# Kernel optimization log

Hardware: AMD Instinct MI355X
Metric: run time of the kernel (lower is better)

Reference implementation:

```python
import jax, jax.numpy as jnp
import numpy as np

B, N, D, H, E = 128, 256, 256, 8, 524288
RATIO = 0.5
HD = D // H
K_SEL = int(N * RATIO)  # nodes kept per graph


def setup_inputs() -> dict:
    key = jax.random.key(0)
    ks = jax.random.split(key, 12)
    embeddings = jax.random.normal(ks[0], (B, N, D), dtype=jnp.float32)
    mask = jnp.ones((B, N), dtype=bool)
    dist = jax.random.uniform(ks[1], (B, N, N), dtype=jnp.float32)
    # within-graph random edges, offset per graph
    epg = E // B
    src = jax.random.randint(ks[2], (B, epg), 0, N)
    dst = jax.random.randint(ks[3], (B, epg), 0, N)
    off = (jnp.arange(B) * N)[:, None]
    edge_index = jnp.stack([(src + off).reshape(-1), (dst + off).reshape(-1)]).astype(jnp.int64)
    batch = jnp.repeat(jnp.arange(B, dtype=jnp.int64), N)
    s = 1.0 / np.sqrt(D)
    Wq = jax.random.normal(ks[4], (D, D), jnp.float32) * s
    Wk = jax.random.normal(ks[5], (D, D), jnp.float32) * s
    Wv = jax.random.normal(ks[6], (D, D), jnp.float32) * s
    Wo = jax.random.normal(ks[7], (D, D), jnp.float32) * s
    bq = jnp.zeros((D,), jnp.float32)
    bk = jnp.zeros((D,), jnp.float32)
    bv = jnp.zeros((D,), jnp.float32)
    bo = jnp.zeros((D,), jnp.float32)
    pool_w = jax.random.normal(ks[8], (D,), jnp.float32) * s
    return dict(embeddings=embeddings, mask=mask, dist=dist, edge_index=edge_index,
                batch=batch, Wq=Wq, bq=bq, Wk=Wk, bk=bk, Wv=Wv, bv=bv, Wo=Wo, bo=bo,
                pool_w=pool_w)


def _mha(x, mask, dist, Wq, bq, Wk, bk, Wv, bv, Wo, bo):
    # x: [B,N,D]; dist used as additive attention bias; mask: [B,N] key mask
    q = (x @ Wq + bq).reshape(B, N, H, HD).transpose(0, 2, 1, 3)  # bhnd
    k = (x @ Wk + bk).reshape(B, N, H, HD).transpose(0, 2, 1, 3)
    v = (x @ Wv + bv).reshape(B, N, H, HD).transpose(0, 2, 1, 3)
    scores = jnp.einsum('bhnd,bhmd->bhnm', q, k) / jnp.sqrt(jnp.float32(HD))
    scores = scores + dist[:, None]  # broadcast bias over heads
    scores = jnp.where(mask[:, None, None, :], scores, jnp.float32(-1e9))
    attn = jax.nn.softmax(scores, axis=-1)
    out = jnp.einsum('bhnm,bhmd->bhnd', attn, v)
    out = out.transpose(0, 2, 1, 3).reshape(B, N, D)
    return out @ Wo + bo


def reference(embeddings, mask, dist, edge_index, batch, Wq, bq, Wk, bk, Wv, bv, Wo, bo, pool_w):
    encoder_result = _mha(embeddings, mask, dist, Wq, bq, Wk, bk, Wv, bv, Wo, bo)
    # encoder_result[mask] -> sparse node features; mask is all-true so shape is [B*N, D]
    x = encoder_result.reshape(B * N, D)

    # ---- TopKPooling (PyG semantics): score = x.w/||w||, keep top ceil(ratio*N)/graph ----
    score = (x @ pool_w) / jnp.linalg.norm(pool_w)          # [B*N]
    vals, idx = jax.lax.top_k(score.reshape(B, N), K_SEL)    # per-graph top-k
    perm = (idx + (jnp.arange(B) * N)[:, None]).reshape(-1)  # [B*K] global node ids
    sub_x = x[perm] * jnp.tanh(vals).reshape(-1, 1)
    sub_batch = batch[perm]

    # relabel nodes: new id = position in perm (PyG ordering); dropped -> sentinel
    n_keep = B * K_SEL
    sentinel = n_keep
    new_id = jnp.full((B * N,), sentinel, dtype=edge_index.dtype).at[perm].set(
        jnp.arange(n_keep, dtype=edge_index.dtype))
    row = new_id[edge_index[0]]
    col = new_id[edge_index[1]]
    valid = (row < sentinel) & (col < sentinel)
    row = jnp.where(valid, row, sentinel)
    col = jnp.where(valid, col, sentinel)
    # sort_edge_index: row-major sort; invalid (sentinel) edges pushed to the end
    order = jnp.argsort(row * (sentinel + 1) + col)
    sub_edge_index = jnp.stack([row, col])[:, order]
    return encoder_result, sub_x, sub_edge_index, sub_batch
```

## Files before the change

kernel.cpp:

```cpp
#include <hip/hip_runtime.h>
#include <math.h>

#define Bg   128
#define Ng   256
#define Dg   256
#define Hg   8
#define HDg  32
#define Eg   524288
#define Kg   128
#define BNg  32768
#define SENT 16384

using bf16x8 = __attribute__((ext_vector_type(8))) short;
using f32x4  = __attribute__((ext_vector_type(4))) float;

__device__ inline void split2(float x, short &h, short &l) {
    unsigned u = __float_as_uint(x);
    h = (short)(u >> 16);
    float hf = __uint_as_float(u & 0xffff0000u);
    float r = x - hf;
    l = (short)(__float_as_uint(r) >> 16);
}
__device__ inline unsigned pack2(short a, short b) {
    return (unsigned)(unsigned short)a | ((unsigned)(unsigned short)b << 16);
}

__global__ __launch_bounds__(256) void split_x(
    const float* __restrict__ x, short* __restrict__ xh, short* __restrict__ xl)
{
    size_t i = ((size_t)blockIdx.x * 256 + threadIdx.x) * 8;
    float4 a = *(const float4*)(x + i);
    float4 b = *(const float4*)(x + i + 4);
    float v[8] = {a.x,a.y,a.z,a.w,b.x,b.y,b.z,b.w};
    short h[8], l[8];
    #pragma unroll
    for (int j = 0; j < 8; ++j) split2(v[j], h[j], l[j]);
    uint4 uh, ul;
    uh.x = pack2(h[0],h[1]); uh.y = pack2(h[2],h[3]);
    uh.z = pack2(h[4],h[5]); uh.w = pack2(h[6],h[7]);
    ul.x = pack2(l[0],l[1]); ul.y = pack2(l[2],l[3]);
    ul.z = pack2(l[4],l[5]); ul.w = pack2(l[6],l[7]);
    *(uint4*)(xh + i) = uh;
    *(uint4*)(xl + i) = ul;
}

__global__ __launch_bounds__(256) void wprep(
    const float* __restrict__ Wq, const float* __restrict__ Wk,
    const float* __restrict__ Wv, const float* __restrict__ Wo,
    short* __restrict__ WTh, short* __restrict__ WTl)
{
    __shared__ float t[64][65];
    const int bid = blockIdx.x;
    const int mat = bid >> 4;
    const int kt = (bid >> 2) & 3, nt = bid & 3;
    const float* W = (mat==0) ? Wq : (mat==1) ? Wk : (mat==2) ? Wv : Wo;
    const int tid = threadIdx.x;
    const int r = tid >> 2, c4 = tid & 3;
    #pragma unroll
    for (int i = 0; i < 4; ++i) {
        float4 v = *(const float4*)(W + (size_t)(kt*64 + r)*256 + nt*64 + c4*16 + i*4);
        t[r][c4*16 + i*4 + 0] = v.x; t[r][c4*16 + i*4 + 1] = v.y;
        t[r][c4*16 + i*4 + 2] = v.z; t[r][c4*16 + i*4 + 3] = v.w;
    }
    __syncthreads();
    const int n = r, k0 = c4 * 16;
    short hb[16], lb[16];
    #pragma unroll
    for (int i = 0; i < 16; ++i) split2(t[k0 + i][n], hb[i], lb[i]);
    size_t base = (size_t)mat*65536 + (size_t)(nt*64 + n)*256 + kt*64 + k0;
    uint4 uh0, uh1, ul0, ul1;
    uh0.x=pack2(hb[0],hb[1]);  uh0.y=pack2(hb[2],hb[3]);  uh0.z=pack2(hb[4],hb[5]);  uh0.w=pack2(hb[6],hb[7]);
    uh1.x=pack2(hb[8],hb[9]);  uh1.y=pack2(hb[10],hb[11]);uh1.z=pack2(hb[12],hb[13]);uh1.w=pack2(hb[14],hb[15]);
    ul0.x=pack2(lb[0],lb[1]);  ul0.y=pack2(lb[2],lb[3]);  ul0.z=pack2(lb[4],lb[5]);  ul0.w=pack2(lb[6],lb[7]);
    ul1.x=pack2(lb[8],lb[9]);  ul1.y=pack2(lb[10],lb[11]);ul1.z=pack2(lb[12],lb[13]);ul1.w=pack2(lb[14],lb[15]);
    *(uint4*)&WTh[base]     = uh0; *(uint4*)&WTh[base + 8] = uh1;
    *(uint4*)&WTl[base]     = ul0; *(uint4*)&WTl[base + 8] = ul1;
}

__global__ __launch_bounds__(256) void qkv_mm(
    const short* __restrict__ xh, const short* __restrict__ xl,
    const short* __restrict__ WTh, const short* __restrict__ WTl,
    const float* __restrict__ bq, const float* __restrict__ bk, const float* __restrict__ bv,
    short* __restrict__ Qh, short* __restrict__ Ql,
    short* __restrict__ Kh, short* __restrict__ Kl,
    short* __restrict__ Vh, short* __restrict__ Vl)
{
    const int z = blockIdx.z;
    const float* bias = (z==0) ? bq : (z==1) ? bk : bv;
    short* outH       = (z==0) ? Qh : (z==1) ? Kh : Vh;
    short* outL       = (z==0) ? Ql : (z==1) ? Kl : Vl;
    const float scale = (z==0) ? 0.17677669529663687f : 1.0f;
    const short* bth = WTh + (size_t)z * 65536;
    const short* btl = WTl + (size_t)z * 65536;
    __shared__ __align__(16) short lds[16384];
    const int tid = threadIdx.x;
    const int lane = tid & 63, w = tid >> 6;
    const int g = lane >> 4, li = lane & 15;
    const int wr = w >> 1, wc = w & 1;
    const int m0 = blockIdx.x * 128, n0 = blockIdx.y * 128;
    f32x4 acc[4][4];
    #pragma unroll
    for (int i = 0; i < 4; ++i)
        #pragma unroll
        for (int j = 0; j < 4; ++j) acc[i][j] = (f32x4){0.f,0.f,0.f,0.f};

    for (int k0 = 0; k0 < 256; k0 += 32) {
        #pragma unroll
        for (int it = 0; it < 2; ++it) {
            int chunk = it*256 + tid;
            int r = chunk >> 2, c = chunk & 3;
            size_t ga = (size_t)(m0 + r)*256 + k0 + c*8;
            size_t gb = (size_t)(n0 + r)*256 + k0 + c*8;
            uint4 vh = *(const uint4*)(xh + ga);
            uint4 vl = *(const uint4*)(xl + ga);
            uint4 wh = *(const uint4*)(bth + gb);
            uint4 wl = *(const uint4*)(btl + gb);
            *(uint4*)&lds[        chunk*8] = vh;
            *(uint4*)&lds[ 4096 + chunk*8] = vl;
            *(uint4*)&lds[ 8192 + chunk*8] = wh;
            *(uint4*)&lds[12288 + chunk*8] = wl;
        }
        __syncthreads();
        bf16x8 ah[4], al[4], bh[4], bl[4];
        #pragma unroll
        for (int i = 0; i < 4; ++i) {
            int row = wr*64 + i*16 + li;
            ah[i] = *(const bf16x8*)&lds[       row*32 + g*8];
            al[i] = *(const bf16x8*)&lds[4096 + row*32 + g*8];
        }
        #pragma unroll
        for (int j = 0; j < 4; ++j) {
            int row = wc*64 + j*16 + li;
            bh[j] = *(const bf16x8*)&lds[ 8192 + row*32 + g*8];
            bl[j] = *(const bf16x8*)&lds[12288 + row*32 + g*8];
        }
        #pragma unroll
        for (int i = 0; i < 4; ++i)
            #pragma unroll
            for (int j = 0; j < 4; ++j) {
                acc[i][j] = __builtin_amdgcn_mfma_f32_16x16x32_bf16(ah[i], bh[j], acc[i][j], 0,0,0);
                acc[i][j] = __builtin_amdgcn_mfma_f32_16x16x32_bf16(ah[i], bl[j], acc[i][j], 0,0,0);
                acc[i][j] = __builtin_amdgcn_mfma_f32_16x16x32_bf16(al[i], bh[j], acc[i][j], 0,0,0);
            }
        __syncthreads();
    }
    #pragma unroll
    for (int i = 0; i < 4; ++i)
        #pragma unroll
        for (int j = 0; j < 4; ++j)
            #pragma unroll
            for (int r = 0; r < 4; ++r) {
                int m = m0 + wr*64 + i*16 + g*4 + r;
                int c = n0 + wc*64 + j*16 + li;
                int b = m >> 8, nn = m & 255;
                int h = c >> 5, hd = c & 31;
                float val = (acc[i][j][r] + bias[c]) * scale;
                short hh, ll; split2(val, hh, ll);
                size_t idx = ((size_t)(b*Hg + h)*Ng + nn)*HDg + hd;
                outH[idx] = hh; outL[idx] = ll;
            }
}

__global__ __launch_bounds__(512, 4) void attn_mfma(
    const short* __restrict__ Qh, const short* __restrict__ Ql,
    const short* __restrict__ Kh, const short* __restrict__ Kl,
    const short* __restrict__ Vh, const short* __restrict__ Vl,
    const float* __restrict__ dist,
    short* __restrict__ AOh, short* __restrict__ AOl)
{
    __shared__ __align__(16) short Khi [2][32][40];
    __shared__ __align__(16) short Klo [2][32][40];
    __shared__ __align__(16) short Vthi[2][32][40];
    __shared__ __align__(16) short Vtlo[2][32][40];
    __shared__ __align__(16) short Phi [8][32][40];
    __shared__ __align__(16) short Plo [8][32][40];

    const int i0 = blockIdx.x;
    const int xcd = i0 & 7;
    const int m_  = i0 >> 3;
    const int h   = m_ & 7;
    const int b   = (m_ >> 3) * 8 + xcd;
    const int bh  = b * 8 + h;

    const int tid = threadIdx.x;
    const int w = tid >> 6;
    const int lane = tid & 63;
    const int g = lane >> 4;
    const int li = lane & 15;
    const int q0 = w * 32;
    const int skey = tid >> 4;
    const int se0  = (tid & 15) * 2;
    const float* dall = dist + (size_t)b*Ng*Ng;

    bf16x8 qh[2], ql[2];
    #pragma unroll
    for (int tq = 0; tq < 2; ++tq) {
        size_t qoff = ((size_t)bh * Ng + q0 + tq*16 + li) * HDg + g*8;
        qh[tq] = *(const bf16x8*)(Qh + qoff);
        ql[tq] = *(const bf16x8*)(Ql + qoff);
    }

    {
        size_t koff = ((size_t)bh*Ng + skey) * HDg + se0;
        unsigned kh1 = *(const unsigned*)(Kh + koff);
        unsigned kl1 = *(const unsigned*)(Kl + koff);
        unsigned vh1 = *(const unsigned*)(Vh + koff);
        unsigned vl1 = *(const unsigned*)(Vl + koff);
        *(unsigned*)&Khi[0][skey][se0] = kh1;
        *(unsigned*)&Klo[0][skey][se0] = kl1;
        Vthi[0][se0+0][skey] = (short)(vh1 & 0xffff);
        Vthi[0][se0+1][skey] = (short)(vh1 >> 16);
        Vtlo[0][se0+0][skey] = (short)(vl1 & 0xffff);
        Vtlo[0][se0+1][skey] = (short)(vl1 >> 16);
    }
    __syncthreads();

    f32x4 O[2][2];
    #pragma unroll
    for (int tq=0;tq<2;++tq)
        #pragma unroll
        for (int td=0;td<2;++td) O[tq][td] = (f32x4){0.f,0.f,0.f,0.f};
    float lpart[2] = {0.f, 0.f};

    for (int ch = 0; ch < 8; ++ch) {
        const int cur = ch & 1;
        const bool pref = (ch < 7);
        unsigned khr, klr, vhr, vlr;
        if (pref) {
            size_t koff = ((size_t)bh*Ng + (ch+1)*32 + skey) * HDg + se0;
            khr = *(const unsigned*)(Kh + koff);
            klr = *(const unsigned*)(Kl + koff);
            vhr = *(const unsigned*)(Vh + koff);
            vlr = *(const unsigned*)(Vl + koff);
        }
        f32x4 sacc[2][2];
        #pragma unroll
        for (int tq = 0; tq < 2; ++tq)
            #pragma unroll
            for (int tc = 0; tc < 2; ++tc) {
                const float* dp = dall + (size_t)(q0 + tq*16 + li)*Ng + ch*32 + tc*16 + g*4;
                float4 dv = *(const float4*)dp;
                sacc[tq][tc] = (f32x4){dv.x, dv.y, dv.z, dv.w};
            }
        bf16x8 kbh[2], kbl[2];
        #pragma unroll
        for (int tc = 0; tc < 2; ++tc) {
            kbh[tc] = *(const bf16x8*)&Khi[cur][tc*16+li][g*8];
            kbl[tc] = *(const bf16x8*)&Klo[cur][tc*16+li][g*8];
        }
        #pragma unroll
        for (int tq = 0; tq < 2; ++tq)
            #pragma unroll
            for (int tc = 0; tc < 2; ++tc) {
                sacc[tq][tc] = __builtin_amdgcn_mfma_f32_16x16x32_bf16(kbh[tc], qh[tq], sacc[tq][tc], 0,0,0);
                sacc[tq][tc] = __builtin_amdgcn_mfma_f32_16x16x32_bf16(kbl[tc], qh[tq], sacc[tq][tc], 0,0,0);
                sacc[tq][tc] = __builtin_amdgcn_mfma_f32_16x16x32_bf16(kbh[tc], ql[tq], sacc[tq][tc], 0,0,0);
            }
        #pragma unroll
        for (int tq = 0; tq < 2; ++tq)
            #pragma unroll
            for (int tc = 0; tc < 2; ++tc) {
                float p0 = __expf(sacc[tq][tc][0] - 16.f);
                float p1 = __expf(sacc[tq][tc][1] - 16.f);
                float p2 = __expf(sacc[tq][tc][2] - 16.f);
                float p3 = __expf(sacc[tq][tc][3] - 16.f);
                lpart[tq] += p0; lpart[tq] += p1; lpart[tq] += p2; lpart[tq] += p3;
                unsigned u0 = __float_as_uint(p0), u1 = __float_as_uint(p1);
                unsigned u2 = __float_as_uint(p2), u3 = __float_as_uint(p3);
                float r0 = p0 - __uint_as_float(u0 & 0xffff0000u);
                float r1 = p1 - __uint_as_float(u1 & 0xffff0000u);
                float r2 = p2 - __uint_as_float(u2 & 0xffff0000u);
                float r3 = p3 - __uint_as_float(u3 & 0xffff0000u);
                uint2 hiq, loq;
                hiq.x = (u0 >> 16) | (u1 & 0xffff0000u);
                hiq.y = (u2 >> 16) | (u3 & 0xffff0000u);
                loq.x = (__float_as_uint(r0) >> 16) | (__float_as_uint(r1) & 0xffff0000u);
                loq.y = (__float_as_uint(r2) >> 16) | (__float_as_uint(r3) & 0xffff0000u);
                *(uint2*)&Phi[w][tq*16 + li][tc*16 + g*4] = hiq;
                *(uint2*)&Plo[w][tq*16 + li][tc*16 + g*4] = loq;
            }
        bf16x8 vbh[2], vbl[2];
        #pragma unroll
        for (int td = 0; td < 2; ++td) {
            vbh[td] = *(const bf16x8*)&Vthi[cur][td*16+li][g*8];
            vbl[td] = *(const bf16x8*)&Vtlo[cur][td*16+li][g*8];
        }
        #pragma unroll
        for (int tq = 0; tq < 2; ++tq) {
            bf16x8 ph = *(const bf16x8*)&Phi[w][tq*16+li][g*8];
            bf16x8 pl = *(const bf16x8*)&Plo[w][tq*16+li][g*8];
            #pragma unroll
            for (int td = 0; td < 2; ++td) {
                O[tq][td] = __builtin_amdgcn_mfma_f32_16x16x32_bf16(vbh[td], ph, O[tq][td], 0,0,0);
                O[tq][td] = __builtin_amdgcn_mfma_f32_16x16x32_bf16(vbl[td], ph, O[tq][td], 0,0,0);
                O[tq][td] = __builtin_amdgcn_mfma_f32_16x16x32_bf16(vbh[td], pl, O[tq][td], 0,0,0);
            }
        }
        if (pref) {
            const int nb = cur ^ 1;
            *(unsigned*)&Khi[nb][skey][se0] = khr;
            *(unsigned*)&Klo[nb][skey][se0] = klr;
            Vthi[nb][se0+0][skey] = (short)(vhr & 0xffff);
            Vthi[nb][se0+1][skey] = (short)(vhr >> 16);
            Vtlo[nb][se0+0][skey] = (short)(vlr & 0xffff);
            Vtlo[nb][se0+1][skey] = (short)(vlr >> 16);
        }
        __syncthreads();
    }
    float inv[2];
    #pragma unroll
    for (int tq = 0; tq < 2; ++tq) {
        float s = lpart[tq];
        s += __shfl_xor(s, 16);
        s += __shfl_xor(s, 32);
        inv[tq] = 1.f / s;
    }
    #pragma unroll
    for (int tq = 0; tq < 2; ++tq)
        #pragma unroll
        for (int td = 0; td < 2; ++td) {
            float v0 = O[tq][td][0] * inv[tq];
            float v1 = O[tq][td][1] * inv[tq];
            float v2 = O[tq][td][2] * inv[tq];
            float v3 = O[tq][td][3] * inv[tq];
            unsigned u0 = __float_as_uint(v0), u1 = __float_as_uint(v1);
            unsigned u2 = __float_as_uint(v2), u3 = __float_as_uint(v3);
            float r0 = v0 - __uint_as_float(u0 & 0xffff0000u);
            float r1 = v1 - __uint_as_float(u1 & 0xffff0000u);
            float r2 = v2 - __uint_as_float(u2 & 0xffff0000u);
            float r3 = v3 - __uint_as_float(u3 & 0xffff0000u);
            uint2 hiq, loq;
            hiq.x = (u0 >> 16) | (u1 & 0xffff0000u);
            hiq.y = (u2 >> 16) | (u3 & 0xffff0000u);
            loq.x = (__float_as_uint(r0) >> 16) | (__float_as_uint(r1) & 0xffff0000u);
            loq.y = (__float_as_uint(r2) >> 16) | (__float_as_uint(r3) & 0xffff0000u);
            int q = q0 + tq*16 + li;
            size_t base = ((size_t)b*Ng + q)*Dg + h*HDg + td*16 + g*4;
            *(uint2*)&AOh[base] = hiq;
            *(uint2*)&AOl[base] = loq;
        }
}

__global__ __launch_bounds__(256) void out_mm(
    const short* __restrict__ aoh, const short* __restrict__ aol,
    const short* __restrict__ bth, const short* __restrict__ btl,
    const float* __restrict__ bo, float* __restrict__ enc)
{
    __shared__ __align__(16) short lds[16384];
    const int tid = threadIdx.x;
    const int lane = tid & 63, w = tid >> 6;
    const int g = lane >> 4, li = lane & 15;
    const int wr = w >> 1, wc = w & 1;
    const int m0 = blockIdx.x * 128, n0 = blockIdx.y * 128;
    f32x4 acc[4][4];
    #pragma unroll
    for (int i = 0; i < 4; ++i)
        #pragma unroll
        for (int j = 0; j < 4; ++j) acc[i][j] = (f32x4){0.f,0.f,0.f,0.f};

    for (int k0 = 0; k0 < 256; k0 += 32) {
        #pragma unroll
        for (int it = 0; it < 2; ++it) {
            int chunk = it*256 + tid;
            int r = chunk >> 2, c = chunk & 3;
            size_t ga = (size_t)(m0 + r)*256 + k0 + c*8;
            size_t gb = (size_t)(n0 + r)*256 + k0 + c*8;
            uint4 ah4 = *(const uint4*)(aoh + ga);
            uint4 al4 = *(const uint4*)(aol + ga);
            uint4 wh  = *(const uint4*)(bth + gb);
            uint4 wl  = *(const uint4*)(btl + gb);
            *(uint4*)&lds[        chunk*8] = ah4;
            *(uint4*)&lds[ 4096 + chunk*8] = al4;
            *(uint4*)&lds[ 8192 + chunk*8] = wh;
            *(uint4*)&lds[12288 + chunk*8] = wl;
        }
        __syncthreads();
        bf16x8 ah[4], al[4], bh[4], bl[4];
        #pragma unroll
        for (int i = 0; i < 4; ++i) {
            int row = wr*64 + i*16 + li;
            ah[i] = *(const bf16x8*)&lds[       row*32 + g*8];
            al[i] = *(const bf16x8*)&lds[4096 + row*32 + g*8];
        }
        #pragma unroll
        for (int j = 0; j < 4; ++j) {
            int row = wc*64 + j*16 + li;
            bh[j] = *(const bf16x8*)&lds[ 8192 + row*32 + g*8];
            bl[j] = *(const bf16x8*)&lds[12288 + row*32 + g*8];
        }
        #pragma unroll
        for (int i = 0; i < 4; ++i)
            #pragma unroll
            for (int j = 0; j < 4; ++j) {
                acc[i][j] = __builtin_amdgcn_mfma_f32_16x16x32_bf16(ah[i], bh[j], acc[i][j], 0,0,0);
                acc[i][j] = __builtin_amdgcn_mfma_f32_16x16x32_bf16(ah[i], bl[j], acc[i][j], 0,0,0);
                acc[i][j] = __builtin_amdgcn_mfma_f32_16x16x32_bf16(al[i], bh[j], acc[i][j], 0,0,0);
            }
        __syncthreads();
    }
    #pragma unroll
    for (int i = 0; i < 4; ++i)
        #pragma unroll
        for (int j = 0; j < 4; ++j)
            #pragma unroll
            for (int r = 0; r < 4; ++r) {
                int m = m0 + wr*64 + i*16 + g*4 + r;
                int c = n0 + wc*64 + j*16 + li;
                enc[(size_t)m*Dg + c] = acc[i][j][r] + bo[c];
            }
}

__global__ __launch_bounds__(256) void score_kernel(
    const float* __restrict__ enc, const float* __restrict__ pw, float* __restrict__ score)
{
    int row  = blockIdx.x * 8 + (threadIdx.x >> 5);
    int lane = threadIdx.x & 31;
    const float* r = enc + (size_t)row * Dg;
    float s = 0.f;
    for (int d = lane; d < Dg; d += 32) s = fmaf(r[d], pw[d], s);
    #pragma unroll
    for (int off = 16; off > 0; off >>= 1) s += __shfl_xor(s, off);
    if (lane == 0) score[row] = s;
}

__global__ void norm_kernel(const float* __restrict__ pw, float* __restrict__ inv_norm)
{
    int t = threadIdx.x;
    float s = 0.f;
    for (int d = t; d < Dg; d += 64) s = fmaf(pw[d], pw[d], s);
    #pragma unroll
    for (int off = 32; off > 0; off >>= 1) s += __shfl_xor(s, off);
    if (t == 0) *inv_norm = 1.0f / sqrtf(s);
}

__global__ __launch_bounds__(256) void topk_kernel(
    const float* __restrict__ score, float* __restrict__ vals, int* __restrict__ idxs,
    int* __restrict__ new_id, float* __restrict__ out_batch)
{
    __shared__ float sh[Ng];
    int bgr = blockIdx.x, t = threadIdx.x;
    float mine = score[(size_t)bgr * Ng + t];
    sh[t] = mine;
    __syncthreads();
    int cnt = 0;
    for (int j = 0; j < Ng; ++j) {
        float v = sh[j];
        cnt += (v > mine || (v == mine && j < t)) ? 1 : 0;
    }
    if (cnt < Kg) {
        int pos = bgr * Kg + cnt;
        vals[pos] = mine;
        idxs[pos] = t;
        new_id[bgr * Ng + t] = pos;
        out_batch[pos] = (float)bgr;
    } else {
        new_id[bgr * Ng + t] = SENT;
    }
}

__global__ __launch_bounds__(256) void subx_kernel(
    const float* __restrict__ enc, const float* __restrict__ vals,
    const int* __restrict__ idxs, const float* __restrict__ inv_norm,
    float* __restrict__ out_subx)
{
    int j    = blockIdx.x * 4 + (threadIdx.x >> 6);
    int lane = threadIdx.x & 63;
    int bgr  = j >> 7;
    int src  = bgr * Ng + idxs[j];
    float scale = tanhf(vals[j] * (*inv_norm));
    float4 v = reinterpret_cast<const float4*>(enc + (size_t)src * Dg)[lane];
    v.x *= scale; v.y *= scale; v.z *= scale; v.w *= scale;
    reinterpret_cast<float4*>(out_subx + (size_t)j * Dg)[lane] = v;
}

__global__ __launch_bounds__(256) void edge_hist(
    const int* __restrict__ ei, const int* __restrict__ new_id, int* __restrict__ counts)
{
    int e = blockIdx.x * 256 + threadIdx.x;
    int r = new_id[ei[e]];
    int c = new_id[ei[Eg + e]];
    if (r != SENT && c != SENT) atomicAdd(&counts[r], 1);
}

__global__ __launch_bounds__(256) void scan_kernel(
    const int* __restrict__ counts, int* __restrict__ offsets)
{
    __shared__ int sums[256];
    int t = threadIdx.x;
    int base = t * 64;
    int s = 0;
    for (int i = 0; i < 64; ++i) s += counts[base + i];
    sums[t] = s;
    __syncthreads();
    for (int off = 1; off < 256; off <<= 1) {
        int add = (t >= off) ? sums[t - off] : 0;
        __syncthreads();
        sums[t] += add;
        __syncthreads();
    }
    int run = sums[t] - s;
    for (int i = 0; i < 64; ++i) { offsets[base + i] = run; run += counts[base + i]; }
    if (t == 255) offsets[SENT] = run;
}

__global__ __launch_bounds__(256) void edge_scatter(
    const int* __restrict__ ei, const int* __restrict__ new_id,
    const int* __restrict__ offsets, int* __restrict__ cursor, int* __restrict__ bucket)
{
    int e = blockIdx.x * 256 + threadIdx.x;
    int r = new_id[ei[e]];
    int c = new_id[ei[Eg + e]];
    if (r != SENT && c != SENT) {
        int pos = offsets[r] + atomicAdd(&cursor[r], 1);
        bucket[pos] = c;
    }
}

__global__ __launch_bounds__(256) void edge_sort_emit(
    const int* __restrict__ offsets, int* bucket, float* __restrict__ out_edges)
{
    int r = blockIdx.x * 256 + threadIdx.x;
    int s = offsets[r], e = offsets[r + 1];
    for (int i = s + 1; i < e; ++i) {
        int key = bucket[i];
        int j = i - 1;
        while (j >= s && bucket[j] > key) { bucket[j+1] = bucket[j]; --j; }
        bucket[j+1] = key;
    }
    float rf = (float)r;
    for (int i = s; i < e; ++i) {
        out_edges[i]      = rf;
        out_edges[Eg + i] = (float)bucket[i];
    }
}

__global__ __launch_bounds__(256) void edge_fill(
    const int* __restrict__ offsets, float* __restrict__ out_edges)
{
    int p = blockIdx.x * 256 + threadIdx.x;
    if (p >= offsets[SENT]) {
        out_edges[p]      = (float)SENT;
        out_edges[Eg + p] = (float)SENT;
    }
}

extern "C" void kernel_launch(void* const* d_in, const int* in_sizes, int n_in,
                              void* d_out, int out_size, void* d_ws, size_t ws_size,
                              hipStream_t stream)
{
    const float* x    = (const float*)d_in[0];
    const float* dist = (const float*)d_in[2];
    const int*   ei   = (const int*)d_in[3];
    const float* Wq = (const float*)d_in[5];
    const float* bq = (const float*)d_in[6];
    const float* Wk = (const float*)d_in[7];
    const float* bk = (const float*)d_in[8];
    const float* Wv = (const float*)d_in[9];
    const float* bv = (const float*)d_in[10];
    const float* Wo = (const float*)d_in[11];
    const float* bo = (const float*)d_in[12];
    const float* pw = (const float*)d_in[13];

    float* out       = (float*)d_out;
    float* enc_out   = out;
    float* subx_out  = out + 8388608;
    float* edge_out  = out + 12582912;
    float* batch_out = out + 13631488;

    float* ws      = (float*)d_ws;
    short* Qh      = (short*)ws;
    short* Ql      = (short*)(ws + 4194304);
    short* Kh      = (short*)(ws + 8388608);
    short* Kl      = (short*)(ws + 12582912);
    short* Vh      = (short*)(ws + 16777216);
    short* Vl      = (short*)(ws + 20971520);
    short* xh      = (short*)(ws + 25165824);
    short* xl      = (short*)(ws + 29360128);
    short* AOh     = xh;
    short* AOl     = xl;
    short* WTh     = (short*)(ws + 33554432);
    short* WTl     = (short*)(ws + 33685504);
    float* score   = ws + 33816576;
    float* vals    = ws + 33849344;
    int*   idxs    = (int*)(ws + 33865728);
    int*   new_id  = (int*)(ws + 33882112);
    int*   counts  = (int*)(ws + 33914880);
    int*   offsets = (int*)(ws + 33931264);
    int*   cursor  = (int*)(ws + 33947680);
    float* inv_nm  = ws + 33964064;
    int*   bucket  = (int*)(ws + 33964096);

    hipMemsetAsync(counts, 0, SENT * sizeof(int), stream);
    hipMemsetAsync(cursor, 0, SENT * sizeof(int), stream);

    split_x       <<<dim3(4096),               256, 0, stream>>>(x, xh, xl);
    wprep         <<<dim3(64),                 256, 0, stream>>>(Wq, Wk, Wv, Wo, WTh, WTl);
    norm_kernel   <<<dim3(1),                   64, 0, stream>>>(pw, inv_nm);
    qkv_mm        <<<dim3(BNg/128, Dg/128, 3), 256, 0, stream>>>(xh, xl, WTh, WTl, bq, bk, bv,
                                                                 Qh, Ql, Kh, Kl, Vh, Vl);
    attn_mfma     <<<dim3(Bg*Hg),              512, 0, stream>>>(Qh, Ql, Kh, Kl, Vh, Vl, dist, AOh, AOl);
    out_mm        <<<dim3(BNg/128, Dg/128),    256, 0, stream>>>(AOh, AOl, WTh + 3*65536, WTl + 3*65536, bo, enc_out);
    score_kernel  <<<dim3(BNg/8),              256, 0, stream>>>(enc_out, pw, score);
    topk_kernel   <<<dim3(Bg),                 256, 0, stream>>>(score, vals, idxs, new_id, batch_out);
    subx_kernel   <<<dim3((Bg*Kg)/4),          256, 0, stream>>>(enc_out, vals, idxs, inv_nm, subx_out);
    edge_hist     <<<dim3(Eg/256),             256, 0, stream>>>(ei, new_id, counts);
    scan_kernel   <<<dim3(1),                  256, 0, stream>>>(counts, offsets);
    edge_scatter  <<<dim3(Eg/256),             256, 0, stream>>>(ei, new_id, offsets, cursor, bucket);
    edge_sort_emit<<<dim3(SENT/256),           256, 0, stream>>>(offsets, bucket, edge_out);
    edge_fill     <<<dim3(Eg/256),             256, 0, stream>>>(offsets, edge_out);
    (void)in_sizes; (void)n_in; (void)out_size; (void)ws_size;
}
```

Before: 232.0 us.

## Double-buffer QKV GEMM LDS tiles and vectorize GEMM epilogue stores

The QKV projection GEMM now uses two LDS buffers and prefetches the next K-slice into registers while MFMAs run on the current one, cutting one barrier per iteration. Both GEMMs (QKV and output projection) swap the MFMA operand order so each lane holds four consecutive output columns. The epilogues can then issue vectorized float4/uint2 stores and float4 bias loads instead of scalar strided writes. This doubles LDS use and adds register pressure from the prefetched values, which could lower occupancy.

```diff
diff --git a/kernel.cpp b/kernel.cpp
--- a/kernel.cpp
+++ b/kernel.cpp
@@ -92,73 +92,108 @@
     const float scale = (z==0) ? 0.17677669529663687f : 1.0f;
     const short* bth = WTh + (size_t)z * 65536;
     const short* btl = WTl + (size_t)z * 65536;
-    __shared__ __align__(16) short lds[16384];
+    __shared__ __align__(16) short lds[2][16384];
     const int tid = threadIdx.x;
     const int lane = tid & 63, w = tid >> 6;
     const int g = lane >> 4, li = lane & 15;
     const int wr = w >> 1, wc = w & 1;
     const int m0 = blockIdx.x * 128, n0 = blockIdx.y * 128;
+    const int sr = tid >> 2, sc = (tid & 3) * 8;
     f32x4 acc[4][4];
     #pragma unroll
     for (int i = 0; i < 4; ++i)
         #pragma unroll
         for (int j = 0; j < 4; ++j) acc[i][j] = (f32x4){0.f,0.f,0.f,0.f};
 
-    for (int k0 = 0; k0 < 256; k0 += 32) {
-        #pragma unroll
-        for (int it = 0; it < 2; ++it) {
-            int chunk = it*256 + tid;
-            int r = chunk >> 2, c = chunk & 3;
-            size_t ga = (size_t)(m0 + r)*256 + k0 + c*8;
-            size_t gb = (size_t)(n0 + r)*256 + k0 + c*8;
-            uint4 vh = *(const uint4*)(xh + ga);
-            uint4 vl = *(const uint4*)(xl + ga);
-            uint4 wh = *(const uint4*)(bth + gb);
-            uint4 wl = *(const uint4*)(btl + gb);
-            *(uint4*)&lds[        chunk*8] = vh;
-            *(uint4*)&lds[ 4096 + chunk*8] = vl;
-            *(uint4*)&lds[ 8192 + chunk*8] = wh;
-            *(uint4*)&lds[12288 + chunk*8] = wl;
-        }
-        __syncthreads();
+    #pragma unroll
+    for (int it = 0; it < 2; ++it) {
+        int chunk = it*256 + tid;
+        int r = chunk >> 2, c = (chunk & 3) * 8;
+        size_t ga = (size_t)(m0 + r)*256 + c;
+        size_t gb = (size_t)(n0 + r)*256 + c;
+        *(uint4*)&lds[0][        chunk*8] = *(const uint4*)(xh + ga);
+        *(uint4*)&lds[0][ 4096 + chunk*8] = *(const uint4*)(xl + ga);
+        *(uint4*)&lds[0][ 8192 + chunk*8] = *(const uint4*)(bth + gb);
+        *(uint4*)&lds[0][12288 + chunk*8] = *(const uint4*)(btl + gb);
+    }
+    __syncthreads();
+
+    for (int k = 0; k < 8; ++k) {
+        const int cur = k & 1;
+        uint4 pf0, pf1, pf2, pf3, pf4, pf5, pf6, pf7;
+        if (k < 7) {
+            int k0n = (k+1)*32;
+            size_t ga0 = (size_t)(m0 + sr)*256 + k0n + sc;
+            size_t gb0 = (size_t)(n0 + sr)*256 + k0n + sc;
+            pf0 = *(const uint4*)(xh + ga0);
+            pf1 = *(const uint4*)(xl + ga0);
+            pf2 = *(const uint4*)(bth + gb0);
+            pf3 = *(const uint4*)(btl + gb0);
+            size_t ga1 = (size_t)(m0 + 64 + sr)*256 + k0n + sc;
+            size_t gb1 = (size_t)(n0 + 64 + sr)*256 + k0n + sc;
+            pf4 = *(const uint4*)(xh + ga1);
+            pf5 = *(const uint4*)(xl + ga1);
+            pf6 = *(const uint4*)(bth + gb1);
+            pf7 = *(const uint4*)(btl + gb1);
+        }
         bf16x8 ah[4], al[4], bh[4], bl[4];
         #pragma unroll
         for (int i = 0; i < 4; ++i) {
             int row = wr*64 + i*16 + li;
-            ah[i] = *(const bf16x8*)&lds[       row*32 + g*8];
-            al[i] = *(const bf16x8*)&lds[4096 + row*32 + g*8];
+            ah[i] = *(const bf16x8*)&lds[cur][       row*32 + g*8];
+            al[i] = *(const bf16x8*)&lds[cur][4096 + row*32 + g*8];
         }
         #pragma unroll
         for (int j = 0; j < 4; ++j) {
             int row = wc*64 + j*16 + li;
-            bh[j] = *(const bf16x8*)&lds[ 8192 + row*32 + g*8];
-            bl[j] = *(const bf16x8*)&lds[12288 + row*32 + g*8];
+            bh[j] = *(const bf16x8*)&lds[cur][ 8192 + row*32 + g*8];
+            bl[j] = *(const bf16x8*)&lds[cur][12288 + row*32 + g*8];
         }
         #pragma unroll
         for (int i = 0; i < 4; ++i)
             #pragma unroll
             for (int j = 0; j < 4; ++j) {
-                acc[i][j] = __builtin_amdgcn_mfma_f32_16x16x32_bf16(ah[i], bh[j], acc[i][j], 0,0,0);
-                acc[i][j] = __builtin_amdgcn_mfma_f32_16x16x32_bf16(ah[i], bl[j], acc[i][j], 0,0,0);
-                acc[i][j] = __builtin_amdgcn_mfma_f32_16x16x32_bf16(al[i], bh[j], acc[i][j], 0,0,0);
+                acc[i][j] = __builtin_amdgcn_mfma_f32_16x16x32_bf16(bh[j], ah[i], acc[i][j], 0,0,0);
+                acc[i][j] = __builtin_amdgcn_mfma_f32_16x16x32_bf16(bl[j], ah[i], acc[i][j], 0,0,0);
+                acc[i][j] = __builtin_amdgcn_mfma_f32_16x16x32_bf16(bh[j], al[i], acc[i][j], 0,0,0);
             }
+        if (k < 7) {
+            const int nb = cur ^ 1;
+            int chunk0 = tid, chunk1 = 256 + tid;
+            *(uint4*)&lds[nb][        chunk0*8] = pf0;
+            *(uint4*)&lds[nb][ 4096 + chunk0*8] = pf1;
+            *(uint4*)&lds[nb][ 8192 + chunk0*8] = pf2;
+            *(uint4*)&lds[nb][12288 + chunk0*8] = pf3;
+            *(uint4*)&lds[nb][        chunk1*8] = pf4;
+            *(uint4*)&lds[nb][ 4096 + chunk1*8] = pf5;
+            *(uint4*)&lds[nb][ 8192 + chunk1*8] = pf6;
+            *(uint4*)&lds[nb][12288 + chunk1*8] = pf7;
+        }
         __syncthreads();
     }
     #pragma unroll
-    for (int i = 0; i < 4; ++i)
-        #pragma unroll
-        for (int j = 0; j < 4; ++j)
-            #pragma unroll
-            for (int r = 0; r < 4; ++r) {
-                int m = m0 + wr*64 + i*16 + g*4 + r;
-                int c = n0 + wc*64 + j*16 + li;
-                int b = m >> 8, nn = m & 255;
-                int h = c >> 5, hd = c & 31;
-                float val = (acc[i][j][r] + bias[c]) * scale;
-                short hh, ll; split2(val, hh, ll);
-                size_t idx = ((size_t)(b*Hg + h)*Ng + nn)*HDg + hd;
-                outH[idx] = hh; outL[idx] = ll;
-            }
+    for (int i = 0; i < 4; ++i) {
+        int mrow = m0 + wr*64 + i*16 + li;
+        int b = mrow >> 8, nn = mrow & 255;
+        #pragma unroll
+        for (int j = 0; j < 4; ++j) {
+            int c0 = n0 + wc*64 + j*16 + g*4;
+            int h = c0 >> 5, hd = c0 & 31;
+            float4 bi = *(const float4*)(bias + c0);
+            float v0 = (acc[i][j][0] + bi.x) * scale;
+            float v1 = (acc[i][j][1] + bi.y) * scale;
+            float v2 = (acc[i][j][2] + bi.z) * scale;
+            float v3 = (acc[i][j][3] + bi.w) * scale;
+            short h0,l0,h1,l1,h2,l2,h3,l3;
+            split2(v0,h0,l0); split2(v1,h1,l1); split2(v2,h2,l2); split2(v3,h3,l3);
+            uint2 hiq, loq;
+            hiq.x = pack2(h0,h1); hiq.y = pack2(h2,h3);
+            loq.x = pack2(l0,l1); loq.y = pack2(l2,l3);
+            size_t idx = ((size_t)(b*Hg + h)*Ng + nn)*HDg + hd;
+            *(uint2*)&outH[idx] = hiq;
+            *(uint2*)&outL[idx] = loq;
+        }
+    }
 }
 
 __global__ __launch_bounds__(512, 4) void attn_mfma(
@@ -392,22 +427,27 @@
         for (int i = 0; i < 4; ++i)
             #pragma unroll
             for (int j = 0; j < 4; ++j) {
-                acc[i][j] = __builtin_amdgcn_mfma_f32_16x16x32_bf16(ah[i], bh[j], acc[i][j], 0,0,0);
-                acc[i][j] = __builtin_amdgcn_mfma_f32_16x16x32_bf16(ah[i], bl[j], acc[i][j], 0,0,0);
-                acc[i][j] = __builtin_amdgcn_mfma_f32_16x16x32_bf16(al[i], bh[j], acc[i][j], 0,0,0);
+                acc[i][j] = __builtin_amdgcn_mfma_f32_16x16x32_bf16(bh[j], ah[i], acc[i][j], 0,0,0);
+                acc[i][j] = __builtin_amdgcn_mfma_f32_16x16x32_bf16(bl[j], ah[i], acc[i][j], 0,0,0);
+                acc[i][j] = __builtin_amdgcn_mfma_f32_16x16x32_bf16(bh[j], al[i], acc[i][j], 0,0,0);
             }
         __syncthreads();
     }
     #pragma unroll
-    for (int i = 0; i < 4; ++i)
-        #pragma unroll
-        for (int j = 0; j < 4; ++j)
-            #pragma unroll
-            for (int r = 0; r < 4; ++r) {
-                int m = m0 + wr*64 + i*16 + g*4 + r;
-                int c = n0 + wc*64 + j*16 + li;
-                enc[(size_t)m*Dg + c] = acc[i][j][r] + bo[c];
-            }
+    for (int i = 0; i < 4; ++i) {
+        int mrow = m0 + wr*64 + i*16 + li;
+        #pragma unroll
+        for (int j = 0; j < 4; ++j) {
+            int c0 = n0 + wc*64 + j*16 + g*4;
+            float4 bo4 = *(const float4*)(bo + c0);
+            float4 v;
+            v.x = acc[i][j][0] + bo4.x;
+            v.y = acc[i][j][1] + bo4.y;
+            v.z = acc[i][j][2] + bo4.z;
+            v.w = acc[i][j][3] + bo4.w;
+            *(float4*)&enc[(size_t)mrow*Dg + c0] = v;
+        }
+    }
 }
 
 __global__ __launch_bounds__(256) void score_kernel(
```

New measurement: 235.9 us. About the same (+1.7%).
